# Performance work log

Hardware: AMD Instinct MI355X
Metric: run time of the kernel (lower is better)

Reference implementation:

```python
import jax, jax.numpy as jnp
import numpy as np


def _gcn_conv(x, edge_index, W, b):
    # PyG GCNConv: h = x @ W; out = D^{-1/2}(A+I)D^{-1/2} h + b
    N = x.shape[0]
    src, dst = edge_index[0], edge_index[1]
    # degree with self-loops (edge weights = 1)
    deg = jax.ops.segment_sum(jnp.ones(src.shape[0], x.dtype), dst, num_segments=N) + 1.0
    dis = jax.lax.rsqrt(deg)  # deg >= 1 so finite
    h = x @ W  # [N, F_out]
    norm = dis[src] * dis[dst]  # [E]
    msg = h[src] * norm[:, None]  # [E, F_out] -- dominant memory traffic
    agg = jax.ops.segment_sum(msg, dst, num_segments=N)
    # self-loop contribution: norm_ii = dis_i^2
    out = agg + h * (dis * dis)[:, None] + b
    return out


def setup_inputs() -> dict:
    key = jax.random.key(0)
    k1, k2, k3, k4, k5, k6 = jax.random.split(key, 6)
    N, E = 100000, 1600000
    in_ch, hid, out_ch = 256, 128, 64  # hid = 2*out_channels
    x = jax.random.normal(k1, (N, in_ch), dtype=jnp.float32)
    edge_index = jax.random.randint(k2, (2, E), 0, N, dtype=jnp.int64)
    # Glorot-style init for GCN weights, zero bias (PyG default)
    W1 = jax.random.normal(k3, (in_ch, hid), dtype=jnp.float32) / np.sqrt(in_ch)
    b1 = jnp.zeros((hid,), jnp.float32)
    W2 = jax.random.normal(k4, (hid, out_ch), dtype=jnp.float32) / np.sqrt(hid)
    b2 = jnp.zeros((out_ch,), jnp.float32)
    return {"x": x, "edge_index": edge_index, "W1": W1, "b1": b1, "W2": W2, "b2": b2}


def reference(x, edge_index, W1, b1, W2, b2):
    # Encoder.forward: k=2 layers of activation(GCNConv(x, edge_index))
    h = jax.nn.relu(_gcn_conv(x, edge_index, W1, b1))
    h = jax.nn.relu(_gcn_conv(h, edge_index, W2, b2))
    return h
```

## Files before the change

kernel.cpp:

```cpp
#include <hip/hip_runtime.h>
#include <math.h>

#define THREADS 256
#define HIST_ILP 8
#define EPB_SHIFT 11

static inline int cdiv(long long a, long long b) { return (int)((a + b - 1) / b); }

typedef __attribute__((ext_vector_type(8))) short bf16x8;
typedef __attribute__((ext_vector_type(4))) float f32x4;

__device__ inline unsigned f2bf_rne_u(float f) {
    unsigned u = __builtin_bit_cast(unsigned, f);
    return (u + 0x7FFFu + ((u >> 16) & 1u)) >> 16;
}
__device__ inline float bfu2f(unsigned h) {
    unsigned u = h << 16;
    return __builtin_bit_cast(float, u);
}


__device__ __forceinline__ void bfrag_unit(const float* __restrict__ W, short* __restrict__ frag,
                                           int NCT, int ctks, int lane) {
    int Nn = NCT * 16;
    int ct = ctks % NCT;
    int ks = ctks / NCT;
    int colc = ct * 16 + (lane & 15);
    int kbase = ks * 32 + (lane >> 4) * 8;
    short* base = frag + (size_t)ctks * 1024 + lane * 8;
    #pragma unroll
    for (int j = 0; j < 8; ++j) {
        float v = W[(size_t)(kbase + j) * Nn + colc];
        unsigned h = f2bf_rne_u(v);
        base[j] = (short)h;
        base[512 + j] = (short)f2bf_rne_u(v - bfu2f(h));
    }
}

template<int NCT, int KS>
__device__ __forceinline__ void gemm_body(const float* __restrict__ A, const short* __restrict__ Bfrag,
                                          unsigned short* __restrict__ H, int M, int blk) {
    constexpr int K = KS * 32;
    constexpr int Nn = NCT * 16;
    const int lane = threadIdx.x & 63;
    const int wave = threadIdx.x >> 6;
    const int rowBase = blk * 128 + wave * 32;
    const int kgrp = (lane >> 4) * 8;

    const float* ap0;
    const float* ap1;
    {
        int r0 = rowBase + (lane & 15);      if (r0 >= M) r0 = M - 1;
        int r1 = rowBase + (lane & 15) + 16; if (r1 >= M) r1 = M - 1;
        ap0 = A + (size_t)r0 * K + kgrp;
        ap1 = A + (size_t)r1 * K + kgrp;
    }

    f32x4 acc[2][NCT] = {};

    float4 c00 = *(const float4*)(ap0);
    float4 c01 = *(const float4*)(ap0 + 4);
    float4 c10 = *(const float4*)(ap1);
    float4 c11 = *(const float4*)(ap1 + 4);

    for (int ks = 0; ks < KS; ++ks) {
        float4 n00, n01, n10, n11;
        if (ks + 1 < KS) {
            const float* p0 = ap0 + (size_t)(ks + 1) * 32;
            const float* p1 = ap1 + (size_t)(ks + 1) * 32;
            n00 = *(const float4*)(p0);
            n01 = *(const float4*)(p0 + 4);
            n10 = *(const float4*)(p1);
            n11 = *(const float4*)(p1 + 4);
        }
        bf16x8 ahi[2], alo[2];
        {
            float av0[8] = {c00.x, c00.y, c00.z, c00.w, c01.x, c01.y, c01.z, c01.w};
            float av1[8] = {c10.x, c10.y, c10.z, c10.w, c11.x, c11.y, c11.z, c11.w};
            #pragma unroll
            for (int j = 0; j < 8; ++j) {
                unsigned h0 = f2bf_rne_u(av0[j]);
                ahi[0][j] = (short)h0;
                alo[0][j] = (short)f2bf_rne_u(av0[j] - bfu2f(h0));
                unsigned h1 = f2bf_rne_u(av1[j]);
                ahi[1][j] = (short)h1;
                alo[1][j] = (short)f2bf_rne_u(av1[j] - bfu2f(h1));
            }
        }
        #pragma unroll
        for (int ct = 0; ct < NCT; ++ct) {
            const short* bp = Bfrag + (size_t)(ks * NCT + ct) * 1024 + lane * 8;
            bf16x8 bhi = *(const bf16x8*)bp;
            bf16x8 blo = *(const bf16x8*)(bp + 512);
            #pragma unroll
            for (int t = 0; t < 2; ++t) {
                acc[t][ct] = __builtin_amdgcn_mfma_f32_16x16x32_bf16(ahi[t], bhi, acc[t][ct], 0, 0, 0);
                acc[t][ct] = __builtin_amdgcn_mfma_f32_16x16x32_bf16(ahi[t], blo, acc[t][ct], 0, 0, 0);
                acc[t][ct] = __builtin_amdgcn_mfma_f32_16x16x32_bf16(alo[t], bhi, acc[t][ct], 0, 0, 0);
            }
        }
        c00 = n00; c01 = n01; c10 = n10; c11 = n11;
    }

    const int drow0 = rowBase + (lane >> 4) * 4;
    #pragma unroll
    for (int t = 0; t < 2; ++t) {
        #pragma unroll
        for (int r = 0; r < 4; ++r) {
            int row = drow0 + t * 16 + r;
            if (row < M) {
                unsigned short* hp = H + (size_t)row * Nn + (lane & 15);
                #pragma unroll
                for (int ct = 0; ct < NCT; ++ct)
                    hp[ct * 16] = (unsigned short)f2bf_rne_u(acc[t][ct][r]);
            }
        }
    }
}


__global__ __launch_bounds__(THREADS)
void zero_bfrag_kernel(int* __restrict__ deg8, int total8,
                       const float* __restrict__ W1, short* __restrict__ bf1,
                       const float* __restrict__ W2, short* __restrict__ bf2, int nbZero) {
    int b = (int)blockIdx.x;
    if (b < nbZero) {
        int base = (b * THREADS + (int)threadIdx.x) * 4;
        if (base + 3 < total8) {
            *(int4*)(deg8 + base) = make_int4(0, 0, 0, 0);
        } else {
            for (int i = base; i < total8; ++i) deg8[i] = 0;
        }
    } else {
        int u = (b - nbZero) * 4 + ((int)threadIdx.x >> 6);
        int lane = threadIdx.x & 63;
        if (u < 64) bfrag_unit(W1, bf1, 8, u, lane);
        else if (u < 80) bfrag_unit(W2, bf2, 4, u - 64, lane);
    }
}

__global__ __launch_bounds__(THREADS)
void hist8_kernel(const int* __restrict__ dst, int* __restrict__ deg8,
                  int* __restrict__ rank, int E, int N) {
    int b = (int)blockIdx.x;
    int* deg = deg8 + (size_t)(b & 7) * N;
    int base = (b << EPB_SHIFT) + (int)threadIdx.x * HIST_ILP;
    if (base + HIST_ILP - 1 < E) {
        int4 d0 = *(const int4*)(dst + base);
        int4 d1 = *(const int4*)(dst + base + 4);
        int4 r0, r1;
        r0.x = atomicAdd(&deg[d0.x], 1);
        r0.y = atomicAdd(&deg[d0.y], 1);
        r0.z = atomicAdd(&deg[d0.z], 1);
        r0.w = atomicAdd(&deg[d0.w], 1);
        r1.x = atomicAdd(&deg[d1.x], 1);
        r1.y = atomicAdd(&deg[d1.y], 1);
        r1.z = atomicAdd(&deg[d1.z], 1);
        r1.w = atomicAdd(&deg[d1.w], 1);
        *(int4*)(rank + base) = r0;
        *(int4*)(rank + base + 4) = r1;
    } else {
        for (int e = base; e < E; ++e) rank[e] = atomicAdd(&deg[dst[e]], 1);
    }
}


#define SCAN_BLOCK 256
#define SCAN_ITEMS 4

__global__ __launch_bounds__(SCAN_BLOCK)
void scan_block_kernel(const int* __restrict__ deg8, int* __restrict__ out,
                       int* __restrict__ blockSums, float* __restrict__ dis, int n) {
    __shared__ int sdata[SCAN_BLOCK];
    int base = blockIdx.x * (SCAN_BLOCK * SCAN_ITEMS);
    int tid = threadIdx.x;
    int v[SCAN_ITEMS];
    int sum = 0;
    #pragma unroll
    for (int k = 0; k < SCAN_ITEMS; ++k) {
        int idx = base + tid * SCAN_ITEMS + k;
        int s8 = 0;
        if (idx < n) {
            #pragma unroll
            for (int c = 0; c < 8; ++c) s8 += deg8[(size_t)c * n + idx];
            dis[idx] = rsqrtf((float)s8 + 1.0f);
        }
        v[k] = s8;
        sum += s8;
    }
    sdata[tid] = sum;
    __syncthreads();
    for (int off = 1; off < SCAN_BLOCK; off <<= 1) {
        int t = (tid >= off) ? sdata[tid - off] : 0;
        __syncthreads();
        sdata[tid] += t;
        __syncthreads();
    }
    if (tid == SCAN_BLOCK - 1) blockSums[blockIdx.x] = sdata[SCAN_BLOCK - 1];
    int run = (tid == 0) ? 0 : sdata[tid - 1];
    #pragma unroll
    for (int k = 0; k < SCAN_ITEMS; ++k) {
        int idx = base + tid * SCAN_ITEMS + k;
        if (idx < n) out[idx] = run;
        run += v[k];
    }
}

__global__ __launch_bounds__(SCAN_BLOCK)
void scan_sums_kernel(int* __restrict__ blockSums, int nB) {
    __shared__ int sdata[SCAN_BLOCK];
    int tid = threadIdx.x;
    sdata[tid] = (tid < nB) ? blockSums[tid] : 0;
    __syncthreads();
    for (int off = 1; off < SCAN_BLOCK; off <<= 1) {
        int t = (tid >= off) ? sdata[tid - off] : 0;
        __syncthreads();
        sdata[tid] += t;
        __syncthreads();
    }
    int excl = (tid == 0) ? 0 : sdata[tid - 1];
    if (tid < nB) blockSums[tid] = excl;
}

__global__ __launch_bounds__(SCAN_BLOCK)
void scan_add_rp8_kernel(int* __restrict__ rowptr, const int* __restrict__ blockSums,
                         const int* __restrict__ deg8, int* __restrict__ rp8,
                         int n, int E) {
    int base = blockIdx.x * (SCAN_BLOCK * SCAN_ITEMS);
    int add = blockSums[blockIdx.x];
    #pragma unroll
    for (int k = 0; k < SCAN_ITEMS; ++k) {
        int idx = base + threadIdx.x * SCAN_ITEMS + k;
        if (idx < n) {
            int val = rowptr[idx] + add;
            rowptr[idx] = val;
            int run = val;
            #pragma unroll
            for (int c = 0; c < 8; ++c) {
                rp8[(size_t)c * n + idx] = run;
                run += deg8[(size_t)c * n + idx];
            }
        }
    }
    if (blockIdx.x == 0 && threadIdx.x == 0) rowptr[n] = E;
}

__global__ __launch_bounds__(THREADS)
void fill_col_rp8_kernel(const int* __restrict__ src, const int* __restrict__ dst,
                         const int* __restrict__ rank, const int* __restrict__ rp8,
                         int* __restrict__ col, int E, int N) {
    int base = ((int)blockIdx.x * THREADS + (int)threadIdx.x) * 4;
    if (base + 3 < E) {
        int c = (base >> EPB_SHIFT) & 7;
        const int* rp = rp8 + (size_t)c * N;
        int4 d = *(const int4*)(dst + base);
        int4 r = *(const int4*)(rank + base);
        int4 s = *(const int4*)(src + base);
        col[rp[d.x] + r.x] = s.x;
        col[rp[d.y] + r.y] = s.y;
        col[rp[d.z] + r.z] = s.z;
        col[rp[d.w] + r.w] = s.w;
    } else {
        for (int e = base; e < E; ++e) {
            int c = (e >> EPB_SHIFT) & 7;
            col[rp8[(size_t)c * N + dst[e]] + rank[e]] = src[e];
        }
    }
}

template<int NCT, int KS>
__global__ __launch_bounds__(THREADS)
void mfma_gemm_bf16out_kernel(const float* __restrict__ A, const short* __restrict__ Bfrag,
                              unsigned short* __restrict__ H, int M) {
    gemm_body<NCT, KS>(A, Bfrag, H, M, (int)blockIdx.x);
}


template<int F, int VEC>
__global__ __launch_bounds__(THREADS)
void gather_bf16_kernel(const unsigned short* __restrict__ g, const int* __restrict__ col,
                        const int* __restrict__ rowptr, const float* __restrict__ dis,
                        const float* __restrict__ bias, float* __restrict__ out, int N) {
    int wid = (int)((blockIdx.x * (long long)blockDim.x + threadIdx.x) >> 6);
    wid = __builtin_amdgcn_readfirstlane(wid);
    const int lane = threadIdx.x & 63;
    if (wid >= N) return;
    const float di = dis[wid];
    const int loff = lane * VEC;

    float acc0 = 0.0f, acc1 = 0.0f;

    auto loadrow = [&](int s) -> unsigned {
        const unsigned short* p = g + (size_t)s * F + loff;
        if (VEC == 2) return *(const unsigned*)p;
        else return (unsigned)*p;
    };
    auto addconv = [&](unsigned u, float w) {
        if (VEC == 2) {
            acc0 += w * bfu2f(u & 0xFFFFu);
            acc1 += w * __builtin_bit_cast(float, u & 0xFFFF0000u);
        } else {
            acc0 += w * bfu2f(u);
        }
    };

    addconv(loadrow(wid), di);

    int start = __builtin_amdgcn_readfirstlane(rowptr[wid]);
    int end   = __builtin_amdgcn_readfirstlane(rowptr[wid + 1]);
    const int* c = col + start;
    int rem = end - start;

    if (rem >= 4) {
        int s0 = __builtin_amdgcn_readfirstlane(c[0]);
        int s1 = __builtin_amdgcn_readfirstlane(c[1]);
        int s2 = __builtin_amdgcn_readfirstlane(c[2]);
        int s3 = __builtin_amdgcn_readfirstlane(c[3]);
        float w0 = dis[s0], w1 = dis[s1], w2 = dis[s2], w3 = dis[s3];
        unsigned u0 = loadrow(s0), u1 = loadrow(s1), u2 = loadrow(s2), u3 = loadrow(s3);
        c += 4; rem -= 4;
        while (rem >= 4) {
            int t0 = __builtin_amdgcn_readfirstlane(c[0]);
            int t1 = __builtin_amdgcn_readfirstlane(c[1]);
            int t2 = __builtin_amdgcn_readfirstlane(c[2]);
            int t3 = __builtin_amdgcn_readfirstlane(c[3]);
            float x0 = dis[t0], x1 = dis[t1], x2 = dis[t2], x3 = dis[t3];
            unsigned v0 = loadrow(t0), v1 = loadrow(t1), v2 = loadrow(t2), v3 = loadrow(t3);
            addconv(u0, w0); addconv(u1, w1); addconv(u2, w2); addconv(u3, w3);
            u0 = v0; u1 = v1; u2 = v2; u3 = v3;
            w0 = x0; w1 = x1; w2 = x2; w3 = x3;
            c += 4; rem -= 4;
        }
        addconv(u0, w0); addconv(u1, w1); addconv(u2, w2); addconv(u3, w3);
    }
    while (rem > 0) {
        int s = __builtin_amdgcn_readfirstlane(c[0]);
        addconv(loadrow(s), dis[s]);
        ++c; --rem;
    }

    float* orow = out + (size_t)wid * F + loff;
    float v0 = di * acc0 + bias[loff];
    if (VEC == 2) {
        float v1 = di * acc1 + bias[loff + 1];
        float2 st = make_float2(fmaxf(v0, 0.0f), fmaxf(v1, 0.0f));
        *(float2*)orow = st;
    } else {
        *orow = fmaxf(v0, 0.0f);
    }
}


#define BM 64
#define BN 64
#define BK 16

__global__ __launch_bounds__(THREADS)
void sgemm_kernel(const float* __restrict__ A, const float* __restrict__ B,
                  float* __restrict__ C, int M, int N, int K) {
    __shared__ float As[BK][BM + 1];
    __shared__ float Bs[BK][BN + 1];

    const int tid = threadIdx.x;
    const int tr = tid / 16;
    const int tc = tid % 16;
    const int rowBase = blockIdx.y * BM;
    const int colBase = blockIdx.x * BN;

    float acc[4][4] = {};

    for (int k0 = 0; k0 < K; k0 += BK) {
        #pragma unroll
        for (int i = tid; i < BM * BK; i += THREADS) {
            int r = i / BK, c = i % BK;
            int gr = rowBase + r;
            As[c][r] = (gr < M) ? A[(size_t)gr * K + k0 + c] : 0.0f;
        }
        #pragma unroll
        for (int i = tid; i < BK * BN; i += THREADS) {
            int r = i / BN, c = i % BN;
            Bs[r][c] = B[(size_t)(k0 + r) * N + colBase + c];
        }
        __syncthreads();

        #pragma unroll
        for (int k = 0; k < BK; ++k) {
            float a[4], b[4];
            #pragma unroll
            for (int m = 0; m < 4; ++m) a[m] = As[k][tr * 4 + m];
            #pragma unroll
            for (int n = 0; n < 4; ++n) b[n] = Bs[k][tc * 4 + n];
            #pragma unroll
            for (int m = 0; m < 4; ++m)
                #pragma unroll
                for (int n = 0; n < 4; ++n)
                    acc[m][n] += a[m] * b[n];
        }
        __syncthreads();
    }

    #pragma unroll
    for (int m = 0; m < 4; ++m) {
        int gr = rowBase + tr * 4 + m;
        if (gr >= M) continue;
        #pragma unroll
        for (int n = 0; n < 4; ++n) {
            C[(size_t)gr * N + colBase + tc * 4 + n] = acc[m][n];
        }
    }
}

__global__ __launch_bounds__(THREADS)
void init_agg_kernel(const float* __restrict__ h, const float* __restrict__ dis,
                     float* __restrict__ agg, int N, int F) {
    int i = blockIdx.x * blockDim.x + threadIdx.x;
    int total = N * (F / 4);
    if (i >= total) return;
    int node = i / (F / 4);
    float d = dis[node];
    float w = d * d;
    float4 v = ((const float4*)h)[i];
    v.x *= w; v.y *= w; v.z *= w; v.w *= w;
    ((float4*)agg)[i] = v;
}

__global__ __launch_bounds__(THREADS)
void edge_scatter_kernel(const float* __restrict__ h, const int* __restrict__ src,
                         const int* __restrict__ dst, const float* __restrict__ dis,
                         float* __restrict__ agg, int E, int F) {
    int lanesPerEdge = F / 4;
    int tid = blockIdx.x * blockDim.x + threadIdx.x;
    int e = tid / lanesPerEdge;
    int c = tid % lanesPerEdge;
    if (e >= E) return;
    int s = src[e];
    int d = dst[e];
    float w = dis[s] * dis[d];
    float4 hv = ((const float4*)(h + (size_t)s * F))[c];
    float* ap = agg + (size_t)d * F + (size_t)c * 4;
    atomicAdd(ap + 0, hv.x * w);
    atomicAdd(ap + 1, hv.y * w);
    atomicAdd(ap + 2, hv.z * w);
    atomicAdd(ap + 3, hv.w * w);
}

__global__ __launch_bounds__(THREADS)
void finalize_kernel(const float* __restrict__ agg, const float* __restrict__ b,
                     float* __restrict__ out, int N, int F) {
    int i = blockIdx.x * blockDim.x + threadIdx.x;
    int total = N * (F / 4);
    if (i >= total) return;
    int c4 = i % (F / 4);
    float4 bv = ((const float4*)b)[c4];
    float4 v = ((const float4*)agg)[i];
    v.x = fmaxf(v.x + bv.x, 0.0f);
    v.y = fmaxf(v.y + bv.y, 0.0f);
    v.z = fmaxf(v.z + bv.z, 0.0f);
    v.w = fmaxf(v.w + bv.w, 0.0f);
    ((float4*)out)[i] = v;
}

__global__ __launch_bounds__(THREADS)
void fdeg_kernel(const int* __restrict__ dst, float* __restrict__ deg, int E) {
    int i = blockIdx.x * blockDim.x + threadIdx.x;
    if (i < E) atomicAdd(&deg[dst[i]], 1.0f);
}

__global__ __launch_bounds__(THREADS)
void fdis_kernel(float* __restrict__ deg, int N) {
    int i = blockIdx.x * blockDim.x + threadIdx.x;
    if (i < N) deg[i] = rsqrtf(deg[i] + 1.0f);
}


extern "C" void kernel_launch(void* const* d_in, const int* in_sizes, int n_in,
                              void* d_out, int out_size, void* d_ws, size_t ws_size,
                              hipStream_t stream) {
    const float* x  = (const float*)d_in[0];
    const int*   ei = (const int*)d_in[1];
    const float* W1 = (const float*)d_in[2];
    const float* b1 = (const float*)d_in[3];
    const float* W2 = (const float*)d_in[4];
    const float* b2 = (const float*)d_in[5];

    const int E    = in_sizes[1] / 2;
    const int hid  = in_sizes[3];
    const int outc = in_sizes[5];
    const int inc  = in_sizes[2] / hid;
    const int N    = in_sizes[0] / inc;

    const int* src = ei;
    const int* dst = ei + E;
    float* out = (float*)d_out;
    char* ws = (char*)d_ws;

    auto al = [](size_t v) { return (v + 255) & ~(size_t)255; };
    size_t o_dis  = 0;
    size_t o_deg8 = al(o_dis + (size_t)N * 4);
    size_t o_rp   = al(o_deg8 + (size_t)N * 32);
    size_t o_rp8  = al(o_rp + ((size_t)N + 1) * 4);
    size_t o_bs   = al(o_rp8 + (size_t)N * 32);
    size_t o_col  = al(o_bs + 4096);
    size_t o_rank = al(o_col + (size_t)E * 4);
    size_t o_bf1  = al(o_rank + (size_t)E * 4);
    size_t o_bf2  = al(o_bf1 + 131072);
    size_t o_G    = al(o_bf2 + 32768);
    size_t o_B    = al(o_G + (size_t)N * hid * 2);
    size_t need   = o_B + (size_t)N * hid * 4;

    if (ws_size >= need && N <= SCAN_BLOCK * SCAN_BLOCK * SCAN_ITEMS &&
        hid == 128 && outc == 64 && inc == 256) {
        float* dis    = (float*)(ws + o_dis);
        int*   deg8   = (int*)(ws + o_deg8);
        int*   rowptr = (int*)(ws + o_rp);
        int*   rp8    = (int*)(ws + o_rp8);
        int*   bsums  = (int*)(ws + o_bs);
        int*   col    = (int*)(ws + o_col);
        int*   rank   = (int*)(ws + o_rank);
        short* bf1    = (short*)(ws + o_bf1);
        short* bf2    = (short*)(ws + o_bf2);
        unsigned short* gbuf = (unsigned short*)(ws + o_G);
        float* out1   = (float*)(ws + o_B);

        const int nbZero  = cdiv((long long)N * 8, 4 * THREADS);
        const int nbHist  = cdiv(E, THREADS * HIST_ILP);
        const int nbGemm1 = cdiv(N, 128);
        const int nbFill  = cdiv(E, 4 * THREADS);

        zero_bfrag_kernel<<<nbZero + 20, THREADS, 0, stream>>>(deg8, N * 8, W1, bf1, W2, bf2, nbZero);

        hist8_kernel<<<nbHist, THREADS, 0, stream>>>(dst, deg8, rank, E, N);

        mfma_gemm_bf16out_kernel<8, 8><<<nbGemm1, THREADS, 0, stream>>>(x, bf1, gbuf, N);

        int nB = cdiv(N, SCAN_BLOCK * SCAN_ITEMS);
        scan_block_kernel<<<nB, SCAN_BLOCK, 0, stream>>>(deg8, rowptr, bsums, dis, N);
        scan_sums_kernel<<<1, SCAN_BLOCK, 0, stream>>>(bsums, nB);
        scan_add_rp8_kernel<<<nB, SCAN_BLOCK, 0, stream>>>(rowptr, bsums, deg8, rp8, N, E);

        fill_col_rp8_kernel<<<nbFill, THREADS, 0, stream>>>(src, dst, rank, rp8, col, E, N);

        gather_bf16_kernel<128, 2><<<cdiv((long long)N * 64, THREADS), THREADS, 0, stream>>>(
            gbuf, col, rowptr, dis, b1, out1, N);

        mfma_gemm_bf16out_kernel<4, 4><<<cdiv(N, 128), THREADS, 0, stream>>>(out1, bf2, gbuf, N);
        gather_bf16_kernel<64, 1><<<cdiv((long long)N * 64, THREADS), THREADS, 0, stream>>>(
            gbuf, col, rowptr, dis, b2, out, N);
        return;
    }

    float* dis = (float*)ws;
    size_t off1 = ((size_t)N * 4 + 255) & ~(size_t)255;
    float* h1 = (float*)(ws + off1);
    size_t off2 = off1 + ((((size_t)N * hid * 4) + 255) & ~(size_t)255);
    float* agg1 = (float*)(ws + off2);
    float* h2   = agg1;
    float* agg2 = agg1 + (size_t)N * outc;

    hipMemsetAsync(dis, 0, (size_t)N * 4, stream);
    fdeg_kernel<<<cdiv(E, THREADS), THREADS, 0, stream>>>(dst, dis, E);
    fdis_kernel<<<cdiv(N, THREADS), THREADS, 0, stream>>>(dis, N);

    {
        dim3 grid(hid / BN, cdiv(N, BM));
        sgemm_kernel<<<grid, THREADS, 0, stream>>>(x, W1, h1, N, hid, inc);
    }
    init_agg_kernel<<<cdiv((long long)N * hid / 4, THREADS), THREADS, 0, stream>>>(h1, dis, agg1, N, hid);
    edge_scatter_kernel<<<cdiv((long long)E * (hid / 4), THREADS), THREADS, 0, stream>>>(
        h1, src, dst, dis, agg1, E, hid);
    finalize_kernel<<<cdiv((long long)N * hid / 4, THREADS), THREADS, 0, stream>>>(agg1, b1, h1, N, hid);

    {
        dim3 grid(outc / BN, cdiv(N, BM));
        sgemm_kernel<<<grid, THREADS, 0, stream>>>(h1, W2, h2, N, outc, hid);
    }
    init_agg_kernel<<<cdiv((long long)N * outc / 4, THREADS), THREADS, 0, stream>>>(h2, dis, agg2, N, outc);
    edge_scatter_kernel<<<cdiv((long long)E * (outc / 4), THREADS), THREADS, 0, stream>>>(
        h2, src, dst, dis, agg2, E, outc);
    finalize_kernel<<<cdiv((long long)N * outc / 4, THREADS), THREADS, 0, stream>>>(agg2, b2, out, N, outc);
}
```

Before: 292.6 us.

## Co-schedule first GEMM with histogram and column-fill kernels, add paired-lane gather

Splits the first-layer MFMA GEMM into two parts. Each part is interleaved, block by block, into the histogram and column-fill launches, so the compute-bound GEMM overlaps the atomic- and scatter-bound graph build. The rank values now carry their histogram copy index in the top 4 bits, so fill no longer depends on the block-to-copy mapping, and the fast path is guarded by E < 2^28. The second-layer gather assigns two half-waves to alternate edges of a row with 32-bit loads and combines them with a shuffle, and MFMA sections raise wave priority. The cost is some load imbalance from the fixed 3:2 GEMM split and extra bit manipulation per edge.

```diff
diff --git a/kernel.cpp b/kernel.cpp
--- a/kernel.cpp
+++ b/kernel.cpp
@@ -37,6 +37,51 @@
     }
 }
 
+__device__ __forceinline__ void hist8_body(const int* __restrict__ dst, int* __restrict__ deg8,
+                                           int* __restrict__ rank, int E, int N,
+                                           int hb, int copy) {
+    int* deg = deg8 + (size_t)copy * N;
+    const int chi = copy << 28;
+    int base = (hb << EPB_SHIFT) + (int)threadIdx.x * HIST_ILP;
+    if (base + HIST_ILP - 1 < E) {
+        int4 d0 = *(const int4*)(dst + base);
+        int4 d1 = *(const int4*)(dst + base + 4);
+        int4 r0, r1;
+        r0.x = atomicAdd(&deg[d0.x], 1) | chi;
+        r0.y = atomicAdd(&deg[d0.y], 1) | chi;
+        r0.z = atomicAdd(&deg[d0.z], 1) | chi;
+        r0.w = atomicAdd(&deg[d0.w], 1) | chi;
+        r1.x = atomicAdd(&deg[d1.x], 1) | chi;
+        r1.y = atomicAdd(&deg[d1.y], 1) | chi;
+        r1.z = atomicAdd(&deg[d1.z], 1) | chi;
+        r1.w = atomicAdd(&deg[d1.w], 1) | chi;
+        *(int4*)(rank + base) = r0;
+        *(int4*)(rank + base + 4) = r1;
+    } else {
+        for (int e = base; e < E; ++e) rank[e] = atomicAdd(&deg[dst[e]], 1) | chi;
+    }
+}
+
+__device__ __forceinline__ void fill_body(const int* __restrict__ src, const int* __restrict__ dst,
+                                          const int* __restrict__ rank, const int* __restrict__ rp8,
+                                          int* __restrict__ col, int E, int N, int blk) {
+    int base = (blk * THREADS + (int)threadIdx.x) * 4;
+    if (base + 3 < E) {
+        int4 d = *(const int4*)(dst + base);
+        int4 r = *(const int4*)(rank + base);
+        int4 s = *(const int4*)(src + base);
+        col[rp8[(size_t)(((unsigned)r.x) >> 28) * N + d.x] + (r.x & 0x0FFFFFFF)] = s.x;
+        col[rp8[(size_t)(((unsigned)r.y) >> 28) * N + d.y] + (r.y & 0x0FFFFFFF)] = s.y;
+        col[rp8[(size_t)(((unsigned)r.z) >> 28) * N + d.z] + (r.z & 0x0FFFFFFF)] = s.z;
+        col[rp8[(size_t)(((unsigned)r.w) >> 28) * N + d.w] + (r.w & 0x0FFFFFFF)] = s.w;
+    } else {
+        for (int e = base; e < E; ++e) {
+            int r = rank[e];
+            col[rp8[(size_t)(((unsigned)r) >> 28) * N + dst[e]] + (r & 0x0FFFFFFF)] = src[e];
+        }
+    }
+}
+
 template<int NCT, int KS>
 __device__ __forceinline__ void gemm_body(const float* __restrict__ A, const short* __restrict__ Bfrag,
                                           unsigned short* __restrict__ H, int M, int blk) {
@@ -87,6 +132,7 @@
                 alo[1][j] = (short)f2bf_rne_u(av1[j] - bfu2f(h1));
             }
         }
+        __builtin_amdgcn_s_setprio(1);
         #pragma unroll
         for (int ct = 0; ct < NCT; ++ct) {
             const short* bp = Bfrag + (size_t)(ks * NCT + ct) * 1024 + lane * 8;
@@ -99,6 +145,7 @@
                 acc[t][ct] = __builtin_amdgcn_mfma_f32_16x16x32_bf16(alo[t], bhi, acc[t][ct], 0, 0, 0);
             }
         }
+        __builtin_amdgcn_s_setprio(0);
         c00 = n00; c01 = n01; c10 = n10; c11 = n11;
     }
 
@@ -140,28 +187,41 @@
 }
 
 __global__ __launch_bounds__(THREADS)
-void hist8_kernel(const int* __restrict__ dst, int* __restrict__ deg8,
-                  int* __restrict__ rank, int E, int N) {
+void hist_gemmA_kernel(const int* __restrict__ dst, int* __restrict__ deg8,
+                       int* __restrict__ rank, int E, int N,
+                       const float* __restrict__ A, const short* __restrict__ Bfrag,
+                       unsigned short* __restrict__ H, int M,
+                       int nbHist, int nbGemm) {
     int b = (int)blockIdx.x;
-    int* deg = deg8 + (size_t)(b & 7) * N;
-    int base = (b << EPB_SHIFT) + (int)threadIdx.x * HIST_ILP;
-    if (base + HIST_ILP - 1 < E) {
-        int4 d0 = *(const int4*)(dst + base);
-        int4 d1 = *(const int4*)(dst + base + 4);
-        int4 r0, r1;
-        r0.x = atomicAdd(&deg[d0.x], 1);
-        r0.y = atomicAdd(&deg[d0.y], 1);
-        r0.z = atomicAdd(&deg[d0.z], 1);
-        r0.w = atomicAdd(&deg[d0.w], 1);
-        r1.x = atomicAdd(&deg[d1.x], 1);
-        r1.y = atomicAdd(&deg[d1.y], 1);
-        r1.z = atomicAdd(&deg[d1.z], 1);
-        r1.w = atomicAdd(&deg[d1.w], 1);
-        *(int4*)(rank + base) = r0;
-        *(int4*)(rank + base + 4) = r1;
-    } else {
-        for (int e = base; e < E; ++e) rank[e] = atomicAdd(&deg[dst[e]], 1);
-    }
+    int total = nbHist + nbGemm;
+    long long t = (long long)b * nbGemm;
+    int gBefore = (int)(t / total);
+    bool isG = (((long long)(b + 1) * nbGemm) / total) > gBefore;
+    if (isG) gemm_body<8, 8>(A, Bfrag, H, M, gBefore);
+    else     hist8_body(dst, deg8, rank, E, N, b - gBefore, b & 7);
+}
+
+__global__ __launch_bounds__(THREADS)
+void fill_gemmB_kernel(const int* __restrict__ src, const int* __restrict__ dst,
+                       const int* __restrict__ rank, const int* __restrict__ rp8,
+                       int* __restrict__ col, int E, int N,
+                       const float* __restrict__ A, const short* __restrict__ Bfrag,
+                       unsigned short* __restrict__ H, int M, int gemmOff,
+                       int nbFill, int nbGemm) {
+    int b = (int)blockIdx.x;
+    int total = nbFill + nbGemm;
+    long long t = (long long)b * nbGemm;
+    int gBefore = (int)(t / total);
+    bool isG = (((long long)(b + 1) * nbGemm) / total) > gBefore;
+    if (isG) gemm_body<8, 8>(A, Bfrag, H, M, gemmOff + gBefore);
+    else     fill_body(src, dst, rank, rp8, col, E, N, b - gBefore);
+}
+
+template<int NCT, int KS>
+__global__ __launch_bounds__(THREADS)
+void mfma_gemm_bf16out_kernel(const float* __restrict__ A, const short* __restrict__ Bfrag,
+                              unsigned short* __restrict__ H, int M) {
+    gemm_body<NCT, KS>(A, Bfrag, H, M, (int)blockIdx.x);
 }
 
 
@@ -245,63 +305,27 @@
     if (blockIdx.x == 0 && threadIdx.x == 0) rowptr[n] = E;
 }
 
-__global__ __launch_bounds__(THREADS)
-void fill_col_rp8_kernel(const int* __restrict__ src, const int* __restrict__ dst,
-                         const int* __restrict__ rank, const int* __restrict__ rp8,
-                         int* __restrict__ col, int E, int N) {
-    int base = ((int)blockIdx.x * THREADS + (int)threadIdx.x) * 4;
-    if (base + 3 < E) {
-        int c = (base >> EPB_SHIFT) & 7;
-        const int* rp = rp8 + (size_t)c * N;
-        int4 d = *(const int4*)(dst + base);
-        int4 r = *(const int4*)(rank + base);
-        int4 s = *(const int4*)(src + base);
-        col[rp[d.x] + r.x] = s.x;
-        col[rp[d.y] + r.y] = s.y;
-        col[rp[d.z] + r.z] = s.z;
-        col[rp[d.w] + r.w] = s.w;
-    } else {
-        for (int e = base; e < E; ++e) {
-            int c = (e >> EPB_SHIFT) & 7;
-            col[rp8[(size_t)c * N + dst[e]] + rank[e]] = src[e];
-        }
-    }
-}
-
-template<int NCT, int KS>
-__global__ __launch_bounds__(THREADS)
-void mfma_gemm_bf16out_kernel(const float* __restrict__ A, const short* __restrict__ Bfrag,
-                              unsigned short* __restrict__ H, int M) {
-    gemm_body<NCT, KS>(A, Bfrag, H, M, (int)blockIdx.x);
-}
-
-
-template<int F, int VEC>
-__global__ __launch_bounds__(THREADS)
-void gather_bf16_kernel(const unsigned short* __restrict__ g, const int* __restrict__ col,
-                        const int* __restrict__ rowptr, const float* __restrict__ dis,
-                        const float* __restrict__ bias, float* __restrict__ out, int N) {
+
+__global__ __launch_bounds__(THREADS)
+void gather_bf16_128_kernel(const unsigned short* __restrict__ g, const int* __restrict__ col,
+                            const int* __restrict__ rowptr, const float* __restrict__ dis,
+                            const float* __restrict__ bias, float* __restrict__ out, int N) {
+    constexpr int F = 128;
     int wid = (int)((blockIdx.x * (long long)blockDim.x + threadIdx.x) >> 6);
     wid = __builtin_amdgcn_readfirstlane(wid);
     const int lane = threadIdx.x & 63;
     if (wid >= N) return;
     const float di = dis[wid];
-    const int loff = lane * VEC;
+    const int loff = lane * 2;
 
     float acc0 = 0.0f, acc1 = 0.0f;
 
     auto loadrow = [&](int s) -> unsigned {
-        const unsigned short* p = g + (size_t)s * F + loff;
-        if (VEC == 2) return *(const unsigned*)p;
-        else return (unsigned)*p;
+        return *(const unsigned*)(g + (size_t)s * F + loff);
     };
     auto addconv = [&](unsigned u, float w) {
-        if (VEC == 2) {
-            acc0 += w * bfu2f(u & 0xFFFFu);
-            acc1 += w * __builtin_bit_cast(float, u & 0xFFFF0000u);
-        } else {
-            acc0 += w * bfu2f(u);
-        }
+        acc0 += w * bfu2f(u & 0xFFFFu);
+        acc1 += w * __builtin_bit_cast(float, u & 0xFFFF0000u);
     };
 
     addconv(loadrow(wid), di);
@@ -341,12 +365,66 @@
 
     float* orow = out + (size_t)wid * F + loff;
     float v0 = di * acc0 + bias[loff];
-    if (VEC == 2) {
-        float v1 = di * acc1 + bias[loff + 1];
-        float2 st = make_float2(fmaxf(v0, 0.0f), fmaxf(v1, 0.0f));
-        *(float2*)orow = st;
-    } else {
-        *orow = fmaxf(v0, 0.0f);
+    float v1 = di * acc1 + bias[loff + 1];
+    *(float2*)orow = make_float2(fmaxf(v0, 0.0f), fmaxf(v1, 0.0f));
+}
+
+__global__ __launch_bounds__(THREADS)
+void gather_pair64_kernel(const unsigned short* __restrict__ g, const int* __restrict__ col,
+                          const int* __restrict__ rowptr, const float* __restrict__ dis,
+                          const float* __restrict__ bias, float* __restrict__ out, int N) {
+    int wid = (int)((blockIdx.x * (long long)blockDim.x + threadIdx.x) >> 6);
+    if (wid >= N) return;
+    const int lane = threadIdx.x & 63;
+    const int half = lane >> 5;
+    const int cc = lane & 31;
+    const float di = dis[wid];
+
+    float acc0 = 0.0f, acc1 = 0.0f;
+
+    auto loadrow = [&](int s) -> unsigned {
+        return *(const unsigned*)(g + (size_t)s * 64 + cc * 2);
+    };
+    auto addconv = [&](unsigned u, float w) {
+        acc0 += w * bfu2f(u & 0xFFFFu);
+        acc1 += w * __builtin_bit_cast(float, u & 0xFFFF0000u);
+    };
+
+    addconv(loadrow(wid), half ? 0.0f : di);
+
+    int start = rowptr[wid], end = rowptr[wid + 1];
+    int j = start + half;
+    int cnt = (j < end) ? ((end - j + 1) >> 1) : 0;
+
+    if (cnt >= 4) {
+        int s0 = col[j], s1 = col[j + 2], s2 = col[j + 4], s3 = col[j + 6];
+        float w0 = dis[s0], w1 = dis[s1], w2 = dis[s2], w3 = dis[s3];
+        unsigned u0 = loadrow(s0), u1 = loadrow(s1), u2 = loadrow(s2), u3 = loadrow(s3);
+        j += 8; cnt -= 4;
+        while (cnt >= 4) {
+            int t0 = col[j], t1 = col[j + 2], t2 = col[j + 4], t3 = col[j + 6];
+            float x0 = dis[t0], x1 = dis[t1], x2 = dis[t2], x3 = dis[t3];
+            unsigned v0 = loadrow(t0), v1 = loadrow(t1), v2 = loadrow(t2), v3 = loadrow(t3);
+            addconv(u0, w0); addconv(u1, w1); addconv(u2, w2); addconv(u3, w3);
+            u0 = v0; u1 = v1; u2 = v2; u3 = v3;
+            w0 = x0; w1 = x1; w2 = x2; w3 = x3;
+            j += 8; cnt -= 4;
+        }
+        addconv(u0, w0); addconv(u1, w1); addconv(u2, w2); addconv(u3, w3);
+    }
+    while (cnt > 0) {
+        int s = col[j];
+        addconv(loadrow(s), dis[s]);
+        j += 2; --cnt;
+    }
+
+    acc0 += __shfl_xor(acc0, 32);
+    acc1 += __shfl_xor(acc1, 32);
+
+    if (half == 0) {
+        float v0 = fmaxf(di * acc0 + bias[cc * 2 + 0], 0.0f);
+        float v1 = fmaxf(di * acc1 + bias[cc * 2 + 1], 0.0f);
+        *(float2*)(out + (size_t)wid * 64 + cc * 2) = make_float2(v0, v1);
     }
 }
 
@@ -509,7 +587,7 @@
     size_t need   = o_B + (size_t)N * hid * 4;
 
     if (ws_size >= need && N <= SCAN_BLOCK * SCAN_BLOCK * SCAN_ITEMS &&
-        hid == 128 && outc == 64 && inc == 256) {
+        hid == 128 && outc == 64 && inc == 256 && E < (1 << 28)) {
         float* dis    = (float*)(ws + o_dis);
         int*   deg8   = (int*)(ws + o_deg8);
         int*   rowptr = (int*)(ws + o_rp);
@@ -525,26 +603,28 @@
         const int nbZero  = cdiv((long long)N * 8, 4 * THREADS);
         const int nbHist  = cdiv(E, THREADS * HIST_ILP);
         const int nbGemm1 = cdiv(N, 128);
+        const int nbGemmA = (nbGemm1 * 3) / 5;
+        const int nbGemmB = nbGemm1 - nbGemmA;
         const int nbFill  = cdiv(E, 4 * THREADS);
 
         zero_bfrag_kernel<<<nbZero + 20, THREADS, 0, stream>>>(deg8, N * 8, W1, bf1, W2, bf2, nbZero);
 
-        hist8_kernel<<<nbHist, THREADS, 0, stream>>>(dst, deg8, rank, E, N);
-
-        mfma_gemm_bf16out_kernel<8, 8><<<nbGemm1, THREADS, 0, stream>>>(x, bf1, gbuf, N);
+        hist_gemmA_kernel<<<nbHist + nbGemmA, THREADS, 0, stream>>>(
+            dst, deg8, rank, E, N, x, bf1, gbuf, N, nbHist, nbGemmA);
 
         int nB = cdiv(N, SCAN_BLOCK * SCAN_ITEMS);
         scan_block_kernel<<<nB, SCAN_BLOCK, 0, stream>>>(deg8, rowptr, bsums, dis, N);
         scan_sums_kernel<<<1, SCAN_BLOCK, 0, stream>>>(bsums, nB);
         scan_add_rp8_kernel<<<nB, SCAN_BLOCK, 0, stream>>>(rowptr, bsums, deg8, rp8, N, E);
 
-        fill_col_rp8_kernel<<<nbFill, THREADS, 0, stream>>>(src, dst, rank, rp8, col, E, N);
-
-        gather_bf16_kernel<128, 2><<<cdiv((long long)N * 64, THREADS), THREADS, 0, stream>>>(
+        fill_gemmB_kernel<<<nbFill + nbGemmB, THREADS, 0, stream>>>(
+            src, dst, rank, rp8, col, E, N, x, bf1, gbuf, N, nbGemmA, nbFill, nbGemmB);
+
+        gather_bf16_128_kernel<<<cdiv((long long)N * 64, THREADS), THREADS, 0, stream>>>(
             gbuf, col, rowptr, dis, b1, out1, N);
 
         mfma_gemm_bf16out_kernel<4, 4><<<cdiv(N, 128), THREADS, 0, stream>>>(out1, bf2, gbuf, N);
-        gather_bf16_kernel<64, 1><<<cdiv((long long)N * 64, THREADS), THREADS, 0, stream>>>(
+        gather_pair64_kernel<<<cdiv((long long)N * 64, THREADS), THREADS, 0, stream>>>(
             gbuf, col, rowptr, dis, b2, out, N);
         return;
     }
```

New measurement: 290.1 us. Within noise of the previous version (-0.8%).
